# Optimization experiments

Hardware: AMD Instinct MI355X
Metric: run time of the kernel (lower is better)

The kernel has to match this reference:

```python
import jax, jax.numpy as jnp
import numpy as np

NT, NB, NY = 1200, 16384, 8
W_LOW, W_HIGH = 0.2, 1.75  # seasonal weights: months 6..9 get W_HIGH


def setup_inputs() -> dict:
    key = jax.random.key(0)
    k1, k2 = jax.random.split(key)
    output = jax.random.normal(k1, (NT, NB, NY), dtype=jnp.float32)
    target = jax.random.normal(k2, (NT, NB, NY), dtype=jnp.float32)
    return {"output": output, "target": target}


def reference(output, target):
    nt = target.shape[0]
    mon = jnp.arange(nt) % 12
    w = jnp.where((mon >= 6) & (mon <= 9), W_HIGH, W_LOW).astype(output.dtype)  # [nt]
    dif = (output - target) * w[:, None, None]  # [nt, nb, ny]
    # per-channel weighted RMSE, summed over channels
    loss = jnp.sqrt(jnp.mean(dif * dif, axis=(0, 1))).sum()
    return loss
```

## Files before the change

### kernel.cpp

```cpp
#include <hip/hip_runtime.h>
#include <hip/hip_bf16.h>
#include <math.h>

#define NT 1200
#define NB 16384
#define NY 8
#define NGROUPS (NT * NB)
#define NQ      (NT * NB * NY / 4)
#define GRID    2048
#define BLOCK   256
#define STRIDE  (GRID * BLOCK)
#define UNROLL  5
#define NITER   15
#define W_LOW  0.2f
#define W_HIGH 1.75f

typedef float f32x4 __attribute__((ext_vector_type(4)));

__global__ __launch_bounds__(BLOCK) void rmse_partial_kernel(
    const float* __restrict__ outp, const float* __restrict__ tgtp,
    float* __restrict__ ws)
{
    const f32x4* __restrict__ o4 = reinterpret_cast<const f32x4*>(outp);
    const f32x4* __restrict__ t4 = reinterpret_cast<const f32x4*>(tgtp);

    const int q0 = blockIdx.x * BLOCK + threadIdx.x;

    f32x4 acc = {0.0f, 0.0f, 0.0f, 0.0f};

#pragma unroll 1
    for (int it = 0; it < NITER; ++it) {
        const int qb = q0 + it * (STRIDE * UNROLL);

        f32x4 a[UNROLL], b[UNROLL];
#pragma unroll
        for (int u = 0; u < UNROLL; ++u) {
            a[u] = o4[qb + u * STRIDE];
            b[u] = t4[qb + u * STRIDE];
        }

#pragma unroll
        for (int u = 0; u < UNROLL; ++u) {
            const int q   = qb + u * STRIDE;
            const int t   = q >> 15;
            const int mon = t % 12;
            const float w2 = (mon >= 6 && mon <= 9) ? (W_HIGH * W_HIGH)
                                                    : (W_LOW * W_LOW);
            f32x4 d = a[u] - b[u];
            acc += (w2 * d) * d;
        }
    }

#pragma unroll
    for (int mask = 2; mask <= 32; mask <<= 1) {
        acc.x += __shfl_xor(acc.x, mask, 64);
        acc.y += __shfl_xor(acc.y, mask, 64);
        acc.z += __shfl_xor(acc.z, mask, 64);
        acc.w += __shfl_xor(acc.w, mask, 64);
    }

    __shared__ float sh[4][NY];
    const int wave = threadIdx.x >> 6;
    const int lane = threadIdx.x & 63;
    if (lane < 2) {
        sh[wave][lane * 4 + 0] = acc.x;
        sh[wave][lane * 4 + 1] = acc.y;
        sh[wave][lane * 4 + 2] = acc.z;
        sh[wave][lane * 4 + 3] = acc.w;
    }
    __syncthreads();

    if (threadIdx.x < NY) {
        const int c = threadIdx.x;
        float s = sh[0][c] + sh[1][c] + sh[2][c] + sh[3][c];
        atomicAdd(&ws[c], s);
    }
}

__global__ void rmse_final_kernel(const float* __restrict__ ws, float* __restrict__ out)
{
    if (threadIdx.x == 0 && blockIdx.x == 0) {
        const float inv_n = 1.0f / (float)NGROUPS;
        float s = 0.0f;
#pragma unroll
        for (int c = 0; c < NY; ++c)
            s += sqrtf(ws[c] * inv_n);
        out[0] = s;
    }
}

extern "C" void kernel_launch(void* const* d_in, const int* in_sizes, int n_in,
                              void* d_out, int out_size, void* d_ws, size_t ws_size,
                              hipStream_t stream) {
    const float* outp = (const float*)d_in[0];
    const float* tgtp = (const float*)d_in[1];
    float* ws  = (float*)d_ws;
    float* out = (float*)d_out;

    (void)hipMemsetAsync(ws, 0, NY * sizeof(float), stream);

    rmse_partial_kernel<<<GRID, BLOCK, 0, stream>>>(outp, tgtp, ws);
    rmse_final_kernel<<<1, 64, 0, stream>>>(ws, out);
}
```

Measured before the change: 266.5 us.

## Give each thread a contiguous 64-byte chunk and split channel accumulators

Each thread now loads four consecutive float4s (two full 8-channel groups) from each input per iteration, instead of single float4s at grid strides. The accumulators become two fixed-channel vectors, which lets the month weight be computed once per chunk and the lane-parity pairing be dropped from the reduction. Grid size drops to 1536 blocks. Per-lane accesses become 64-byte strided, which may hurt coalescing relative to the previous unit-stride float4 pattern.

```diff
diff --git a/kernel.cpp b/kernel.cpp
--- a/kernel.cpp
+++ b/kernel.cpp
@@ -7,11 +7,11 @@
 #define NY 8
 #define NGROUPS (NT * NB)
 #define NQ      (NT * NB * NY / 4)
-#define GRID    2048
+#define GRID    1536
 #define BLOCK   256
-#define STRIDE  (GRID * BLOCK)
-#define UNROLL  5
-#define NITER   15
+#define NTHREADS (GRID * BLOCK)
+#define CHUNK   4
+#define NITER   (NQ / (NTHREADS * CHUNK))
 #define W_LOW  0.2f
 #define W_HIGH 1.75f
 
@@ -24,56 +24,67 @@
     const f32x4* __restrict__ o4 = reinterpret_cast<const f32x4*>(outp);
     const f32x4* __restrict__ t4 = reinterpret_cast<const f32x4*>(tgtp);
 
-    const int q0 = blockIdx.x * BLOCK + threadIdx.x;
+    const int c0 = blockIdx.x * BLOCK + threadIdx.x;
 
-    f32x4 acc = {0.0f, 0.0f, 0.0f, 0.0f};
+    f32x4 accA = {0.0f, 0.0f, 0.0f, 0.0f};
+    f32x4 accB = {0.0f, 0.0f, 0.0f, 0.0f};
 
 #pragma unroll 1
     for (int it = 0; it < NITER; ++it) {
-        const int qb = q0 + it * (STRIDE * UNROLL);
+        const int c   = c0 + it * NTHREADS;
+        const int qb  = c << 2;
+        const int t   = c >> 13;
+        const int mon = t % 12;
+        const float w2 = (mon >= 6 && mon <= 9) ? (W_HIGH * W_HIGH)
+                                                : (W_LOW * W_LOW);
 
-        f32x4 a[UNROLL], b[UNROLL];
-#pragma unroll
-        for (int u = 0; u < UNROLL; ++u) {
-            a[u] = o4[qb + u * STRIDE];
-            b[u] = t4[qb + u * STRIDE];
-        }
+        f32x4 a0 = o4[qb + 0];
+        f32x4 a1 = o4[qb + 1];
+        f32x4 a2 = o4[qb + 2];
+        f32x4 a3 = o4[qb + 3];
+        f32x4 b0 = t4[qb + 0];
+        f32x4 b1 = t4[qb + 1];
+        f32x4 b2 = t4[qb + 2];
+        f32x4 b3 = t4[qb + 3];
 
-#pragma unroll
-        for (int u = 0; u < UNROLL; ++u) {
-            const int q   = qb + u * STRIDE;
-            const int t   = q >> 15;
-            const int mon = t % 12;
-            const float w2 = (mon >= 6 && mon <= 9) ? (W_HIGH * W_HIGH)
-                                                    : (W_LOW * W_LOW);
-            f32x4 d = a[u] - b[u];
-            acc += (w2 * d) * d;
-        }
+        f32x4 d0 = a0 - b0;
+        f32x4 d1 = a1 - b1;
+        f32x4 d2 = a2 - b2;
+        f32x4 d3 = a3 - b3;
+
+        accA += (w2 * d0) * d0;
+        accB += (w2 * d1) * d1;
+        accA += (w2 * d2) * d2;
+        accB += (w2 * d3) * d3;
     }
 
 #pragma unroll
-    for (int mask = 2; mask <= 32; mask <<= 1) {
-        acc.x += __shfl_xor(acc.x, mask, 64);
-        acc.y += __shfl_xor(acc.y, mask, 64);
-        acc.z += __shfl_xor(acc.z, mask, 64);
-        acc.w += __shfl_xor(acc.w, mask, 64);
+    for (int mask = 1; mask <= 32; mask <<= 1) {
+        accA.x += __shfl_xor(accA.x, mask, 64);
+        accA.y += __shfl_xor(accA.y, mask, 64);
+        accA.z += __shfl_xor(accA.z, mask, 64);
+        accA.w += __shfl_xor(accA.w, mask, 64);
+        accB.x += __shfl_xor(accB.x, mask, 64);
+        accB.y += __shfl_xor(accB.y, mask, 64);
+        accB.z += __shfl_xor(accB.z, mask, 64);
+        accB.w += __shfl_xor(accB.w, mask, 64);
     }
 
     __shared__ float sh[4][NY];
     const int wave = threadIdx.x >> 6;
     const int lane = threadIdx.x & 63;
-    if (lane < 2) {
-        sh[wave][lane * 4 + 0] = acc.x;
-        sh[wave][lane * 4 + 1] = acc.y;
-        sh[wave][lane * 4 + 2] = acc.z;
-        sh[wave][lane * 4 + 3] = acc.w;
+    if (lane == 0) {
+        sh[wave][0] = accA.x; sh[wave][1] = accA.y;
+        sh[wave][2] = accA.z; sh[wave][3] = accA.w;
+        sh[wave][4] = accB.x; sh[wave][5] = accB.y;
+        sh[wave][6] = accB.z; sh[wave][7] = accB.w;
     }
     __syncthreads();
 
     if (threadIdx.x < NY) {
-        const int c = threadIdx.x;
-        float s = sh[0][c] + sh[1][c] + sh[2][c] + sh[3][c];
-        atomicAdd(&ws[c], s);
+        const int ch = threadIdx.x;
+        float s = sh[0][ch] + sh[1][ch] + sh[2][ch] + sh[3][ch];
+        atomicAdd(&ws[ch], s);
     }
 }
 
```

Result: faster. 213.6 us (-19.9%).
